# Kernel optimization log

Measured on AMD Instinct MI355X. Metric: run time of the kernel, lower is better.

## Reference

```python
import jax, jax.numpy as jnp
import numpy as np

CH_IN = 256
CA = CH_IN // 8   # attention channels (theta/phi)
CH = CH_IN // 2   # value channels (g)


def _maxpool2(t):
    # 2x2 max pool, stride 2: (B,C,H,W) -> (B,C,H//2,W//2)
    b, c, h, w = t.shape
    return t.reshape(b, c, h // 2, 2, w // 2, 2).max(axis=(3, 5))


def setup_inputs() -> dict:
    key = jax.random.key(0)
    ks = jax.random.split(key, 6)
    B, H, W = 16, 64, 64
    x = jax.random.normal(ks[0], (B, CH_IN, H, W), dtype=jnp.float32)
    # 1x1 conv weights stored as (out_ch, in_ch); spectral_norm is a weight
    # reparameterization, so the forward math is a plain conv with these weights.
    s = 0.05
    w_theta = jax.random.normal(ks[1], (CA, CH_IN), dtype=jnp.float32) * s
    w_phi = jax.random.normal(ks[2], (CA, CH_IN), dtype=jnp.float32) * s
    w_g = jax.random.normal(ks[3], (CH, CH_IN), dtype=jnp.float32) * s
    w_o = jax.random.normal(ks[4], (CH_IN, CH), dtype=jnp.float32) * s
    # gamma is initialized to 0 in the module; use a nonzero value so the
    # attention branch contributes to the output.
    gamma = jnp.asarray(0.5, dtype=jnp.float32)
    return {"x": x, "w_theta": w_theta, "w_phi": w_phi, "w_g": w_g,
            "w_o": w_o, "gamma": gamma}


def reference(x, w_theta, w_phi, w_g, w_o, gamma):
    B, C, H, W = x.shape
    # 1x1 convs as channel contractions
    theta = jnp.einsum('oc,bchw->bohw', w_theta, x)            # (B,CA,H,W)
    phi = _maxpool2(jnp.einsum('oc,bchw->bohw', w_phi, x))     # (B,CA,H/2,W/2)
    g = _maxpool2(jnp.einsum('oc,bchw->bohw', w_g, x))         # (B,CH,H/2,W/2)
    N = H * W
    M = N // 4
    theta = theta.reshape(B, CA, N)
    phi = phi.reshape(B, CA, M)
    g = g.reshape(B, CH, M)
    # beta = softmax(theta^T phi) over keys (no scaling, as in original)
    beta = jax.nn.softmax(jnp.einsum('bcn,bcm->bnm', theta, phi), axis=-1)  # (B,N,M)
    o = jnp.einsum('bcm,bnm->bcn', g, beta).reshape(B, CH, H, W)
    o = jnp.einsum('oc,bchw->bohw', w_o, o)                    # (B,C,H,W)
    return gamma * o + x
```

## Files before the change

### kernel.cpp

```cpp
#include <hip/hip_runtime.h>
#include <hip/hip_bf16.h>

#define NB 16
#define CIN 256
#define CA 32
#define CH 128
#define NN 4096
#define MM 1024

typedef __attribute__((ext_vector_type(8))) short s16x8;
typedef __attribute__((ext_vector_type(4))) float f32x4;

static __device__ __forceinline__ unsigned short f2bf(float x) {
  __hip_bfloat16 h = __float2bfloat16(x);
  return __builtin_bit_cast(unsigned short, h);
}
static __device__ __forceinline__ float bf2f(unsigned short u) {
  unsigned int v = ((unsigned int)u) << 16;
  return __builtin_bit_cast(float, v);
}
static __device__ __forceinline__ unsigned int pk2(float a, float b) {
  return (unsigned)f2bf(a) | ((unsigned)f2bf(b) << 16);
}
static __device__ __forceinline__ void gload_lds16(const void* g, void* s) {
  __builtin_amdgcn_global_load_lds(
      (const __attribute__((address_space(1))) unsigned int*)g,
      (__attribute__((address_space(3))) unsigned int*)s, 16, 0, 0);
}

__global__ __launch_bounds__(256) void k_wcvt(const float* __restrict__ w_theta,
                                              const float* __restrict__ w_phi,
                                              const float* __restrict__ w_g,
                                              const float* __restrict__ w_o,
                                              unsigned short* __restrict__ wcat2,
                                              unsigned short* __restrict__ wo2) {
  const int i = blockIdx.x * 256 + threadIdx.x;
  if (i < 49152) {
    const int row = i >> 8, c = i & 255;
    const float v = (row < 32) ? w_theta[i]
                  : (row < 64) ? w_phi[i - 8192]
                               : w_g[i - 16384];
    const int dst = ((row >> 4) * 8 + (c >> 5)) * 512 +
                    (((c >> 3) & 3) * 16 + (row & 15)) * 8 + (c & 7);
    wcat2[dst] = f2bf(v);
  } else {
    const int w = i - 49152;
    const int c_out = w >> 7, k = w & 127;
    const int dst = (((c_out >> 4) * 16) + ((k >> 5) * 4) + ((k >> 3) & 3)) * 128 +
                    ((c_out & 15) << 3) + (k & 7);
    wo2[dst] = f2bf(w_o[w]);
  }
}

__global__ __launch_bounds__(512) void k_proj(const float* __restrict__ x,
                                              const unsigned short* __restrict__ wcat2,
                                              unsigned short* __restrict__ theta,
                                              unsigned short* __restrict__ phi2,
                                              unsigned short* __restrict__ g2) {
  __shared__ unsigned short xl[32][140];
  __shared__ unsigned short ol[192][136];
  const int b = blockIdx.y;
  const int t = blockIdx.x;
  const int tid = threadIdx.x;
  const int wv = tid >> 6;
  const int l = tid & 63;
  const int grp = l >> 4, col = l & 15;
  const float* xb = x + (size_t)b * CIN * NN;
  f32x4 acc[12];
#pragma unroll
  for (int r = 0; r < 12; ++r) acc[r] = f32x4{0.f, 0.f, 0.f, 0.f};
#pragma unroll 1
  for (int kc = 0; kc < 8; ++kc) {
#pragma unroll
    for (int s = 0; s < 2; ++s) {
      const int i = tid + s * 512;
      const int cl = i >> 5, nq = i & 31;
      const float4 v = *reinterpret_cast<const float4*>(
          xb + (size_t)(kc * 32 + cl) * NN + t * 128 + nq * 4);
      *reinterpret_cast<uint2*>(&xl[cl][nq * 4]) =
          make_uint2(pk2(v.x, v.y), pk2(v.z, v.w));
    }
    __syncthreads();
    s16x8 bfrag;
#pragma unroll
    for (int j = 0; j < 8; ++j)
      bfrag[j] = (short)xl[grp * 8 + j][wv * 16 + col];
#pragma unroll
    for (int r = 0; r < 12; ++r) {
      const s16x8 af = *reinterpret_cast<const s16x8*>(
          wcat2 + (size_t)(r * 8 + kc) * 512 + l * 8);
      acc[r] = __builtin_amdgcn_mfma_f32_16x16x32_bf16(af, bfrag, acc[r], 0, 0, 0);
    }
    __syncthreads();
  }
#pragma unroll
  for (int r = 0; r < 12; ++r)
#pragma unroll
    for (int q = 0; q < 4; ++q)
      ol[r * 16 + grp * 4 + q][wv * 16 + col] = f2bf(acc[r][q]);
  __syncthreads();
  unsigned short* thb = theta + (size_t)b * NN * CA;
  for (int i = tid; i < 128 * 16; i += 512) {
    const int n = i >> 4, cp = (i & 15) << 1;
    const unsigned int v = (unsigned)ol[cp][n] | ((unsigned)ol[cp + 1][n] << 16);
    *reinterpret_cast<unsigned int*>(thb + (size_t)(t * 128 + n) * CA + cp) = v;
  }
  unsigned short* phb2 = phi2 + (size_t)b * MM * CA;
  for (int i = tid; i < 32 * 32; i += 512) {
    const int ca = i & 31, mx = i >> 5;
    const float v = fmaxf(
        fmaxf(bf2f(ol[32 + ca][2 * mx]), bf2f(ol[32 + ca][2 * mx + 1])),
        fmaxf(bf2f(ol[32 + ca][64 + 2 * mx]), bf2f(ol[32 + ca][64 + 2 * mx + 1])));
    const int m = t * 32 + mx;
    phb2[(m >> 4) * 512 + (ca >> 3) * 128 + (m & 15) * 8 + (ca & 7)] = f2bf(v);
  }
  unsigned short* gb2 = g2 + (size_t)b * CH * MM;
  for (int i = tid; i < 128 * 32; i += 512) {
    const int mx = i & 31, c = i >> 5;
    const float v = fmaxf(
        fmaxf(bf2f(ol[64 + c][2 * mx]), bf2f(ol[64 + c][2 * mx + 1])),
        fmaxf(bf2f(ol[64 + c][64 + 2 * mx]), bf2f(ol[64 + c][64 + 2 * mx + 1])));
    const int pg = (mx & 15) >> 2;
    const int pj = (mx & 3) | ((mx >> 4) << 2);
    gb2[(size_t)(t * 8 + (c >> 4)) * 512 + pg * 128 + (c & 15) * 8 + pj] = f2bf(v);
  }
}

__global__ __launch_bounds__(256, 3) void k_attn_out(
    const unsigned short* __restrict__ theta, const unsigned short* __restrict__ phi2,
    const unsigned short* __restrict__ g2, const unsigned short* __restrict__ wo2,
    const float* __restrict__ x, const float* __restrict__ gammap,
    float* __restrict__ out) {
  __shared__ __align__(16) unsigned short kv[2][10240];
  const int b = blockIdx.y;
  const int tid = threadIdx.x;
  const int wv = tid >> 6;
  const int l = tid & 63;
  const int grp = l >> 4, col = l & 15;
  const int n0 = blockIdx.x * 128 + wv * 32;
  const unsigned short* thb = theta + (size_t)b * NN * CA;
  const unsigned short* ph2b = phi2 + (size_t)b * MM * CA;
  const unsigned short* gb2 = g2 + (size_t)b * CH * MM;
  const s16x8 qf0 = *reinterpret_cast<const s16x8*>(thb + (size_t)(n0 + col) * CA + grp * 8);
  const s16x8 qf1 = *reinterpret_cast<const s16x8*>(thb + (size_t)(n0 + 16 + col) * CA + grp * 8);

  auto STAGE = [&](int buf, int tile) {
    const int mc = tile * 64;
    const unsigned short* ksrc = ph2b + (mc >> 4) * 512;
    const unsigned short* vsrc = gb2 + (size_t)(mc >> 5) * 4096;
#pragma unroll
    for (int q = 0; q < 5; ++q) {
      const int i = wv * 5 + q;
      const unsigned short* src = (i < 4) ? (ksrc + i * 512) : (vsrc + (size_t)(i - 4) * 512);
      gload_lds16(src + (size_t)l * 8, &kv[buf][i * 512]);
    }
  };

  f32x4 oa0[8], oa1[8];
#pragma unroll
  for (int t = 0; t < 8; ++t) {
    oa0[t] = f32x4{0.f, 0.f, 0.f, 0.f};
    oa1[t] = f32x4{0.f, 0.f, 0.f, 0.f};
  }
  float m0 = -INFINITY, l0 = 0.f, m1 = -INFINITY, l1 = 0.f;
  const f32x4 z4 = {0.f, 0.f, 0.f, 0.f};

  STAGE(0, 0);
  __syncthreads();
#pragma unroll 1
  for (int it = 0; it < 16; ++it) {
    const int cur = it & 1;
    if (it < 15) STAGE(cur ^ 1, it + 1);
    const unsigned short* kb = &kv[cur][0];
    const unsigned short* vb = &kv[cur][2048];
    const int fo = grp * 128 + col * 8;
    const s16x8 kf0 = *reinterpret_cast<const s16x8*>(kb + 0 * 512 + fo);
    const s16x8 kf1 = *reinterpret_cast<const s16x8*>(kb + 1 * 512 + fo);
    const s16x8 kf2 = *reinterpret_cast<const s16x8*>(kb + 2 * 512 + fo);
    const s16x8 kf3 = *reinterpret_cast<const s16x8*>(kb + 3 * 512 + fo);
    f32x4 s00 = __builtin_amdgcn_mfma_f32_16x16x32_bf16(kf0, qf0, z4, 0, 0, 0);
    f32x4 s01 = __builtin_amdgcn_mfma_f32_16x16x32_bf16(kf1, qf0, z4, 0, 0, 0);
    f32x4 s02 = __builtin_amdgcn_mfma_f32_16x16x32_bf16(kf2, qf0, z4, 0, 0, 0);
    f32x4 s03 = __builtin_amdgcn_mfma_f32_16x16x32_bf16(kf3, qf0, z4, 0, 0, 0);
    f32x4 s10 = __builtin_amdgcn_mfma_f32_16x16x32_bf16(kf0, qf1, z4, 0, 0, 0);
    f32x4 s11 = __builtin_amdgcn_mfma_f32_16x16x32_bf16(kf1, qf1, z4, 0, 0, 0);
    f32x4 s12 = __builtin_amdgcn_mfma_f32_16x16x32_bf16(kf2, qf1, z4, 0, 0, 0);
    f32x4 s13 = __builtin_amdgcn_mfma_f32_16x16x32_bf16(kf3, qf1, z4, 0, 0, 0);
    float cm0 = -INFINITY, cm1 = -INFINITY;
#pragma unroll
    for (int r = 0; r < 4; ++r) {
      cm0 = fmaxf(cm0, fmaxf(fmaxf(s00[r], s01[r]), fmaxf(s02[r], s03[r])));
      cm1 = fmaxf(cm1, fmaxf(fmaxf(s10[r], s11[r]), fmaxf(s12[r], s13[r])));
    }
    cm0 = fmaxf(cm0, __shfl_xor(cm0, 16));
    cm0 = fmaxf(cm0, __shfl_xor(cm0, 32));
    cm1 = fmaxf(cm1, __shfl_xor(cm1, 16));
    cm1 = fmaxf(cm1, __shfl_xor(cm1, 32));
    if (!__all(cm0 <= m0 + 8.f && cm1 <= m1 + 8.f)) {
      const float mn0 = fmaxf(m0, cm0), mn1 = fmaxf(m1, cm1);
      const float sc0 = __expf(m0 - mn0), sc1 = __expf(m1 - mn1);
      l0 *= sc0;
      l1 *= sc1;
#pragma unroll
      for (int t = 0; t < 8; ++t) {
#pragma unroll
        for (int r = 0; r < 4; ++r) {
          oa0[t][r] *= sc0;
          oa1[t][r] *= sc1;
        }
      }
      m0 = mn0;
      m1 = mn1;
    }
    s16x8 pfA0, pfB0, pfA1, pfB1;
    {
      float p0[4], p1[4], p2[4], p3[4];
      float cs = 0.f;
#pragma unroll
      for (int r = 0; r < 4; ++r) {
        p0[r] = __expf(s00[r] - m0);
        p1[r] = __expf(s01[r] - m0);
        p2[r] = __expf(s02[r] - m0);
        p3[r] = __expf(s03[r] - m0);
        cs += (p0[r] + p1[r]) + (p2[r] + p3[r]);
      }
      cs += __shfl_xor(cs, 16);
      cs += __shfl_xor(cs, 32);
      l0 += cs;
      const uint4 ua = make_uint4(pk2(p0[0], p0[1]), pk2(p0[2], p0[3]),
                                  pk2(p1[0], p1[1]), pk2(p1[2], p1[3]));
      const uint4 ub = make_uint4(pk2(p2[0], p2[1]), pk2(p2[2], p2[3]),
                                  pk2(p3[0], p3[1]), pk2(p3[2], p3[3]));
      pfA0 = __builtin_bit_cast(s16x8, ua);
      pfB0 = __builtin_bit_cast(s16x8, ub);
    }
    {
      float p0[4], p1[4], p2[4], p3[4];
      float cs = 0.f;
#pragma unroll
      for (int r = 0; r < 4; ++r) {
        p0[r] = __expf(s10[r] - m1);
        p1[r] = __expf(s11[r] - m1);
        p2[r] = __expf(s12[r] - m1);
        p3[r] = __expf(s13[r] - m1);
        cs += (p0[r] + p1[r]) + (p2[r] + p3[r]);
      }
      cs += __shfl_xor(cs, 16);
      cs += __shfl_xor(cs, 32);
      l1 += cs;
      const uint4 ua = make_uint4(pk2(p0[0], p0[1]), pk2(p0[2], p0[3]),
                                  pk2(p1[0], p1[1]), pk2(p1[2], p1[3]));
      const uint4 ub = make_uint4(pk2(p2[0], p2[1]), pk2(p2[2], p2[3]),
                                  pk2(p3[0], p3[1]), pk2(p3[2], p3[3]));
      pfA1 = __builtin_bit_cast(s16x8, ua);
      pfB1 = __builtin_bit_cast(s16x8, ub);
    }
#pragma unroll
    for (int t = 0; t < 8; ++t) {
      const s16x8 vfA = *reinterpret_cast<const s16x8*>(vb + t * 512 + fo);
      const s16x8 vfB = *reinterpret_cast<const s16x8*>(vb + 4096 + t * 512 + fo);
      oa0[t] = __builtin_amdgcn_mfma_f32_16x16x32_bf16(vfA, pfA0, oa0[t], 0, 0, 0);
      oa0[t] = __builtin_amdgcn_mfma_f32_16x16x32_bf16(vfB, pfB0, oa0[t], 0, 0, 0);
      oa1[t] = __builtin_amdgcn_mfma_f32_16x16x32_bf16(vfA, pfA1, oa1[t], 0, 0, 0);
      oa1[t] = __builtin_amdgcn_mfma_f32_16x16x32_bf16(vfB, pfB1, oa1[t], 0, 0, 0);
    }
    __syncthreads();
  }
  unsigned short* obw = &kv[0][0] + (size_t)wv * (32 * 136);
  const float ri0 = 1.f / l0, ri1 = 1.f / l1;
#pragma unroll
  for (int t = 0; t < 8; ++t) {
    *reinterpret_cast<uint2*>(obw + col * 136 + t * 16 + grp * 4) =
        make_uint2(pk2(oa0[t][0] * ri0, oa0[t][1] * ri0),
                   pk2(oa0[t][2] * ri0, oa0[t][3] * ri0));
    *reinterpret_cast<uint2*>(obw + (16 + col) * 136 + t * 16 + grp * 4) =
        make_uint2(pk2(oa1[t][0] * ri1, oa1[t][1] * ri1),
                   pk2(oa1[t][2] * ri1, oa1[t][3] * ri1));
  }
  s16x8 of0[4], of1[4];
#pragma unroll
  for (int ks = 0; ks < 4; ++ks) {
    of0[ks] = *reinterpret_cast<const s16x8*>(obw + col * 136 + ks * 32 + grp * 8);
    of1[ks] = *reinterpret_cast<const s16x8*>(obw + (16 + col) * 136 + ks * 32 + grp * 8);
  }
  const float gamma = gammap[0];
  const float* xb2 = x + (size_t)b * CIN * NN;
  float* outb = out + (size_t)b * CIN * NN;
#pragma unroll 1
  for (int t2 = 0; t2 < 16; ++t2) {
    f32x4 a20 = {0.f, 0.f, 0.f, 0.f};
    f32x4 a21 = {0.f, 0.f, 0.f, 0.f};
#pragma unroll
    for (int ks = 0; ks < 4; ++ks) {
      const s16x8 wf = *reinterpret_cast<const s16x8*>(
          wo2 + (size_t)(t2 * 16 + ks * 4 + grp) * 128 + col * 8);
      a20 = __builtin_amdgcn_mfma_f32_16x16x32_bf16(wf, of0[ks], a20, 0, 0, 0);
      a21 = __builtin_amdgcn_mfma_f32_16x16x32_bf16(wf, of1[ks], a21, 0, 0, 0);
    }
#pragma unroll
    for (int r = 0; r < 4; ++r) {
      const size_t idx = (size_t)(t2 * 16 + grp * 4 + r) * NN + n0 + col;
      outb[idx] = fmaf(gamma, a20[r], xb2[idx]);
      outb[idx + 16] = fmaf(gamma, a21[r], xb2[idx + 16]);
    }
  }
}

extern "C" void kernel_launch(void* const* d_in, const int* in_sizes, int n_in,
                              void* d_out, int out_size, void* d_ws, size_t ws_size,
                              hipStream_t stream) {
  const float* x = (const float*)d_in[0];
  const float* w_theta = (const float*)d_in[1];
  const float* w_phi = (const float*)d_in[2];
  const float* w_g = (const float*)d_in[3];
  const float* w_o = (const float*)d_in[4];
  const float* gamma = (const float*)d_in[5];
  float* out = (float*)d_out;
  char* ws = (char*)d_ws;
  unsigned short* theta = (unsigned short*)(ws + 0);
  unsigned short* phi2 = (unsigned short*)(ws + 4194304);
  unsigned short* g2 = (unsigned short*)(ws + 5242880);
  unsigned short* wo2 = (unsigned short*)(ws + 9437184);
  unsigned short* wcat2 = (unsigned short*)(ws + 9502720);

  k_wcvt<<<dim3(320), 256, 0, stream>>>(w_theta, w_phi, w_g, w_o, wcat2, wo2);
  k_proj<<<dim3(NN / 128, NB), 512, 0, stream>>>(x, wcat2, theta, phi2, g2);
  k_attn_out<<<dim3(NN / 128, NB), 256, 0, stream>>>(theta, phi2, g2, wo2, x, gamma, out);
}
```

Baseline: 85.04 us.

## Give each wave private K/V buffers and drop block barriers in attention loop

The attention kernel now uses 2-wave blocks, and each wave stages its own key/value tiles into a private LDS region with a two-deep prefetch. Waits use explicit vmcnt counts instead of __syncthreads, so the block-wide barrier per iteration goes away. Tiles shrink from 64 to 32 keys, doubling the iteration count. Each wave now loads every K/V tile itself instead of sharing them across four waves, which multiplies global/L2 traffic. The epilogue, not fully shown here, may still rely on cross-wave LDS reuse that the removed barrier used to order.

```diff
diff --git a/kernel.cpp b/kernel.cpp
--- a/kernel.cpp
+++ b/kernel.cpp
@@ -126,33 +126,34 @@
   }
 }
 
-__global__ __launch_bounds__(256, 3) void k_attn_out(
+__global__ __launch_bounds__(128, 2) void k_attn_out(
     const unsigned short* __restrict__ theta, const unsigned short* __restrict__ phi2,
     const unsigned short* __restrict__ g2, const unsigned short* __restrict__ wo2,
     const float* __restrict__ x, const float* __restrict__ gammap,
     float* __restrict__ out) {
-  __shared__ __align__(16) unsigned short kv[2][10240];
+  __shared__ __align__(16) unsigned short kv[2 * 2 * 5120];
   const int b = blockIdx.y;
   const int tid = threadIdx.x;
   const int wv = tid >> 6;
   const int l = tid & 63;
   const int grp = l >> 4, col = l & 15;
-  const int n0 = blockIdx.x * 128 + wv * 32;
+  const int n0 = blockIdx.x * 64 + wv * 32;
   const unsigned short* thb = theta + (size_t)b * NN * CA;
   const unsigned short* ph2b = phi2 + (size_t)b * MM * CA;
   const unsigned short* gb2 = g2 + (size_t)b * CH * MM;
+  unsigned short* kvw = &kv[wv * 10240];
   const s16x8 qf0 = *reinterpret_cast<const s16x8*>(thb + (size_t)(n0 + col) * CA + grp * 8);
   const s16x8 qf1 = *reinterpret_cast<const s16x8*>(thb + (size_t)(n0 + 16 + col) * CA + grp * 8);
 
   auto STAGE = [&](int buf, int tile) {
-    const int mc = tile * 64;
+    const int mc = tile * 32;
     const unsigned short* ksrc = ph2b + (mc >> 4) * 512;
     const unsigned short* vsrc = gb2 + (size_t)(mc >> 5) * 4096;
-#pragma unroll
-    for (int q = 0; q < 5; ++q) {
-      const int i = wv * 5 + q;
-      const unsigned short* src = (i < 4) ? (ksrc + i * 512) : (vsrc + (size_t)(i - 4) * 512);
-      gload_lds16(src + (size_t)l * 8, &kv[buf][i * 512]);
+    unsigned short* dst = kvw + buf * 5120;
+#pragma unroll
+    for (int q = 0; q < 10; ++q) {
+      const unsigned short* src = (q < 2) ? (ksrc + q * 512) : (vsrc + (size_t)(q - 2) * 512);
+      gload_lds16(src + (size_t)l * 8, dst + q * 512);
     }
   };
 
@@ -166,31 +167,29 @@
   const f32x4 z4 = {0.f, 0.f, 0.f, 0.f};
 
   STAGE(0, 0);
-  __syncthreads();
+  STAGE(1, 1);
 #pragma unroll 1
-  for (int it = 0; it < 16; ++it) {
+  for (int it = 0; it < 32; ++it) {
     const int cur = it & 1;
-    if (it < 15) STAGE(cur ^ 1, it + 1);
-    const unsigned short* kb = &kv[cur][0];
-    const unsigned short* vb = &kv[cur][2048];
+    if (it < 31) {
+      asm volatile("s_waitcnt vmcnt(10)" ::: "memory");
+    } else {
+      asm volatile("s_waitcnt vmcnt(0)" ::: "memory");
+    }
+    const unsigned short* kb = kvw + cur * 5120;
+    const unsigned short* vb = kb + 1024;
     const int fo = grp * 128 + col * 8;
-    const s16x8 kf0 = *reinterpret_cast<const s16x8*>(kb + 0 * 512 + fo);
-    const s16x8 kf1 = *reinterpret_cast<const s16x8*>(kb + 1 * 512 + fo);
-    const s16x8 kf2 = *reinterpret_cast<const s16x8*>(kb + 2 * 512 + fo);
-    const s16x8 kf3 = *reinterpret_cast<const s16x8*>(kb + 3 * 512 + fo);
+    const s16x8 kf0 = *reinterpret_cast<const s16x8*>(kb + fo);
+    const s16x8 kf1 = *reinterpret_cast<const s16x8*>(kb + 512 + fo);
     f32x4 s00 = __builtin_amdgcn_mfma_f32_16x16x32_bf16(kf0, qf0, z4, 0, 0, 0);
     f32x4 s01 = __builtin_amdgcn_mfma_f32_16x16x32_bf16(kf1, qf0, z4, 0, 0, 0);
-    f32x4 s02 = __builtin_amdgcn_mfma_f32_16x16x32_bf16(kf2, qf0, z4, 0, 0, 0);
-    f32x4 s03 = __builtin_amdgcn_mfma_f32_16x16x32_bf16(kf3, qf0, z4, 0, 0, 0);
     f32x4 s10 = __builtin_amdgcn_mfma_f32_16x16x32_bf16(kf0, qf1, z4, 0, 0, 0);
     f32x4 s11 = __builtin_amdgcn_mfma_f32_16x16x32_bf16(kf1, qf1, z4, 0, 0, 0);
-    f32x4 s12 = __builtin_amdgcn_mfma_f32_16x16x32_bf16(kf2, qf1, z4, 0, 0, 0);
-    f32x4 s13 = __builtin_amdgcn_mfma_f32_16x16x32_bf16(kf3, qf1, z4, 0, 0, 0);
     float cm0 = -INFINITY, cm1 = -INFINITY;
 #pragma unroll
     for (int r = 0; r < 4; ++r) {
-      cm0 = fmaxf(cm0, fmaxf(fmaxf(s00[r], s01[r]), fmaxf(s02[r], s03[r])));
-      cm1 = fmaxf(cm1, fmaxf(fmaxf(s10[r], s11[r]), fmaxf(s12[r], s13[r])));
+      cm0 = fmaxf(cm0, fmaxf(s00[r], s01[r]));
+      cm1 = fmaxf(cm1, fmaxf(s10[r], s11[r]));
     }
     cm0 = fmaxf(cm0, __shfl_xor(cm0, 16));
     cm0 = fmaxf(cm0, __shfl_xor(cm0, 32));
@@ -212,61 +211,48 @@
       m0 = mn0;
       m1 = mn1;
     }
-    s16x8 pfA0, pfB0, pfA1, pfB1;
+    s16x8 pf0, pf1;
     {
-      float p0[4], p1[4], p2[4], p3[4];
+      float p0[4], p1[4];
       float cs = 0.f;
 #pragma unroll
       for (int r = 0; r < 4; ++r) {
         p0[r] = __expf(s00[r] - m0);
         p1[r] = __expf(s01[r] - m0);
-        p2[r] = __expf(s02[r] - m0);
-        p3[r] = __expf(s03[r] - m0);
-        cs += (p0[r] + p1[r]) + (p2[r] + p3[r]);
+        cs += p0[r] + p1[r];
       }
       cs += __shfl_xor(cs, 16);
       cs += __shfl_xor(cs, 32);
       l0 += cs;
       const uint4 ua = make_uint4(pk2(p0[0], p0[1]), pk2(p0[2], p0[3]),
                                   pk2(p1[0], p1[1]), pk2(p1[2], p1[3]));
-      const uint4 ub = make_uint4(pk2(p2[0], p2[1]), pk2(p2[2], p2[3]),
-                                  pk2(p3[0], p3[1]), pk2(p3[2], p3[3]));
-      pfA0 = __builtin_bit_cast(s16x8, ua);
-      pfB0 = __builtin_bit_cast(s16x8, ub);
+      pf0 = __builtin_bit_cast(s16x8, ua);
     }
     {
-      float p0[4], p1[4], p2[4], p3[4];
+      float p0[4], p1[4];
       float cs = 0.f;
 #pragma unroll
       for (int r = 0; r < 4; ++r) {
         p0[r] = __expf(s10[r] - m1);
         p1[r] = __expf(s11[r] - m1);
-        p2[r] = __expf(s12[r] - m1);
-        p3[r] = __expf(s13[r] - m1);
-        cs += (p0[r] + p1[r]) + (p2[r] + p3[r]);
+        cs += p0[r] + p1[r];
       }
       cs += __shfl_xor(cs, 16);
       cs += __shfl_xor(cs, 32);
       l1 += cs;
       const uint4 ua = make_uint4(pk2(p0[0], p0[1]), pk2(p0[2], p0[3]),
                                   pk2(p1[0], p1[1]), pk2(p1[2], p1[3]));
-      const uint4 ub = make_uint4(pk2(p2[0], p2[1]), pk2(p2[2], p2[3]),
-                                  pk2(p3[0], p3[1]), pk2(p3[2], p3[3]));
-      pfA1 = __builtin_bit_cast(s16x8, ua);
-      pfB1 = __builtin_bit_cast(s16x8, ub);
+      pf1 = __builtin_bit_cast(s16x8, ua);
     }
 #pragma unroll
     for (int t = 0; t < 8; ++t) {
       const s16x8 vfA = *reinterpret_cast<const s16x8*>(vb + t * 512 + fo);
-      const s16x8 vfB = *reinterpret_cast<const s16x8*>(vb + 4096 + t * 512 + fo);
-      oa0[t] = __builtin_amdgcn_mfma_f32_16x16x32_bf16(vfA, pfA0, oa0[t], 0, 0, 0);
-      oa0[t] = __builtin_amdgcn_mfma_f32_16x16x32_bf16(vfB, pfB0, oa0[t], 0, 0, 0);
-      oa1[t] = __builtin_amdgcn_mfma_f32_16x16x32_bf16(vfA, pfA1, oa1[t], 0, 0, 0);
-      oa1[t] = __builtin_amdgcn_mfma_f32_16x16x32_bf16(vfB, pfB1, oa1[t], 0, 0, 0);
-    }
-    __syncthreads();
-  }
-  unsigned short* obw = &kv[0][0] + (size_t)wv * (32 * 136);
+      oa0[t] = __builtin_amdgcn_mfma_f32_16x16x32_bf16(vfA, pf0, oa0[t], 0, 0, 0);
+      oa1[t] = __builtin_amdgcn_mfma_f32_16x16x32_bf16(vfA, pf1, oa1[t], 0, 0, 0);
+    }
+    if (it < 30) STAGE(cur, it + 2);
+  }
+  unsigned short* obw = kvw;
   const float ri0 = 1.f / l0, ri1 = 1.f / l1;
 #pragma unroll
   for (int t = 0; t < 8; ++t) {
@@ -325,5 +311,5 @@
 
   k_wcvt<<<dim3(320), 256, 0, stream>>>(w_theta, w_phi, w_g, w_o, wcat2, wo2);
   k_proj<<<dim3(NN / 128, NB), 512, 0, stream>>>(x, wcat2, theta, phi2, g2);
-  k_attn_out<<<dim3(NN / 128, NB), 256, 0, stream>>>(theta, phi2, g2, wo2, x, gamma, out);
-}
+  k_attn_out<<<dim3(NN / 64, NB), 128, 0, stream>>>(theta, phi2, g2, wo2, x, gamma, out);
+}
```

New measurement: 97.57 us. 1.15x slower.
